# Performance work log

Hardware: AMD Instinct MI355X
Metric: run time of the kernel (lower is better)

The kernel has to match this reference:

```python
import jax, jax.numpy as jnp
import numpy as np

T, B, I, H = 1024, 64, 3, 2048


def setup_inputs() -> dict:
    key = jax.random.key(0)
    ks = jax.random.split(key, 6)
    lim = 1.0 / np.sqrt(H).astype(np.float32)  # eqx GRUCell init range
    return {
        "inp": jax.random.normal(ks[0], (T, B, I), jnp.float32),
        "init_hidden": jax.random.normal(ks[1], (B, H), jnp.float32),
        "weight_ih": jax.random.uniform(ks[2], (3 * H, I), jnp.float32, -lim, lim),
        "weight_hh": jax.random.uniform(ks[3], (3 * H, H), jnp.float32, -lim, lim),
        "bias": jax.random.uniform(ks[4], (3 * H,), jnp.float32, -lim, lim),
        "bias_n": jax.random.uniform(ks[5], (H,), jnp.float32, -lim, lim),
    }


def reference(inp, init_hidden, weight_ih, weight_hh, bias, bias_n):
    # Input projections for all timesteps at once: [T, B, 3H]
    igates_all = jnp.einsum("tbi,gi->tbg", inp, weight_ih) + bias

    def step(h, ig):
        hg = h @ weight_hh.T  # [B, 3H]
        ig_r, ig_z, ig_n = jnp.split(ig, 3, axis=-1)
        hg_r, hg_z, hg_n = jnp.split(hg, 3, axis=-1)
        reset = jax.nn.sigmoid(ig_r + hg_r)
        upd = jax.nn.sigmoid(ig_z + hg_z)
        new = jnp.tanh(ig_n + reset * (hg_n + bias_n))
        h_new = new + upd * (h - new)  # eqx GRUCell: new + inp_gate*(hidden-new)
        return h_new, h_new[:, 0]      # out = first hidden unit per step

    _, out = jax.lax.scan(step, init_hidden, igates_all)
    return out  # [T, B]
```

## Files before the change

kernel.cpp:

```cpp
#include <hip/hip_runtime.h>

typedef __attribute__((ext_vector_type(8))) short bf16x8;
typedef __attribute__((ext_vector_type(4))) float f32x4;
typedef __attribute__((ext_vector_type(4))) int i32x4;

#define Tn 1024
#define Bn 64
#define Hn 2048
#define NBLK 256
#define NTHR 512

#define GRP(ring, leaf, g) (((((ring) << 7) | ((leaf) << 3) | (g))) * 32)

#define SPIN_LIMIT (1u << 25)

__device__ __forceinline__ unsigned short f2b(float x) {
    unsigned u = __float_as_uint(x);
    return (unsigned short)((u + 0x7fffu + ((u >> 16) & 1u)) >> 16);
}
__device__ __forceinline__ float sigm(float x) {
    return __builtin_amdgcn_rcpf(1.0f + __expf(-x));
}
__device__ __forceinline__ float tanh_f(float x) {
    float e = __expf(2.0f * x);
    return 1.0f - 2.0f * __builtin_amdgcn_rcpf(1.0f + e);
}

__device__ __forceinline__ void store_short_wt(unsigned short* p, unsigned v) {
    asm volatile("global_store_short %0, %1, off sc0 sc1" :: "v"(p), "v"(v) : "memory");
}
__device__ __forceinline__ void store_dword_wt(float* p, float v) {
    asm volatile("global_store_dword %0, %1, off sc0 sc1" :: "v"(p), "v"(__float_as_uint(v)) : "memory");
}
__device__ __forceinline__ void store_u64_wt(unsigned long long* p, unsigned long long v) {
    asm volatile("global_store_dwordx2 %0, %1, off sc0 sc1" :: "v"(p), "v"(v) : "memory");
}
__device__ __forceinline__ unsigned poll_read(unsigned* p) {
    unsigned old;
    asm volatile("global_atomic_add %0, %1, %2, off sc0 sc1\n\ts_waitcnt vmcnt(0)"
                 : "=v"(old) : "v"(p), "v"(0u) : "memory");
    return old;
}

__device__ __forceinline__ long hfrag_off(int b, int k) {
    return ((long)(((k >> 5) * 4 + (b >> 4)) * 64) + ((k >> 3) & 3) * 16 + (b & 15)) * 8 + (k & 7);
}

__global__ void prep_kernel(const float* __restrict__ init_h,
                            unsigned short* __restrict__ h0,
                            unsigned* __restrict__ ctrl) {
    const int i = blockIdx.x * 256 + threadIdx.x;
    const int b  = i >> 9;
    const int k4 = (i & 511) << 2;
    float4 v = *reinterpret_cast<const float4*>(init_h + (long)b * Hn + k4);
    unsigned long long q = (unsigned long long)f2b(v.x)
                         | ((unsigned long long)f2b(v.y) << 16)
                         | ((unsigned long long)f2b(v.z) << 32)
                         | ((unsigned long long)f2b(v.w) << 48);
    store_u64_wt((unsigned long long*)(h0 + hfrag_off(b, k4)), q);
    if (i < 8192)
        asm volatile("global_store_dword %0, %1, off sc0 sc1"
                     :: "v"(ctrl + i), "v"(0u) : "memory");
}

__global__ void __launch_bounds__(NTHR, 2) gru_kernel(
    const float* __restrict__ inp,
    const float* __restrict__ init_h,
    const float* __restrict__ w_ih,
    const float* __restrict__ w_hh,
    const float* __restrict__ bias,
    const float* __restrict__ bias_n,
    unsigned short* __restrict__ h0,
    unsigned short* __restrict__ h1,
    unsigned* __restrict__ ctrl,
    float* __restrict__ out)
{
    __shared__ f32x4 red[2][4][2][3][64];

    const int tid  = threadIdx.x;
    const int lane = tid & 63;
    const int w    = tid >> 6;
    const int quad = lane >> 4;
    const int n16  = lane & 15;
    const int R    = blockIdx.x & 1;
    const int c    = blockIdx.x >> 1;
    const int jg   = c * 16 + n16;
    const int ks   = w * 256;
    const int bbase = 32 * R;

    bf16x8 Bf[3][8];
    #pragma unroll
    for (int nt = 0; nt < 3; ++nt) {
        const long row = (long)(nt * Hn + jg);
        #pragma unroll
        for (int k = 0; k < 8; ++k) {
            const float* p = w_hh + row * Hn + ks + k * 32 + quad * 8;
            bf16x8 b;
            #pragma unroll
            for (int j = 0; j < 8; ++j) b[j] = (short)f2b(p[j]);
            Bf[nt][k] = b;
        }
    }

    float wr0 = w_ih[jg*3+0], wr1 = w_ih[jg*3+1], wr2 = w_ih[jg*3+2];
    float wz0 = w_ih[(Hn+jg)*3+0], wz1 = w_ih[(Hn+jg)*3+1], wz2 = w_ih[(Hn+jg)*3+2];
    float wn0 = w_ih[(2*Hn+jg)*3+0], wn1 = w_ih[(2*Hn+jg)*3+1], wn2 = w_ih[(2*Hn+jg)*3+2];
    float br_ = bias[jg], bz_ = bias[Hn+jg], bn2_ = bias[2*Hn+jg];
    float bnn_ = bias_n[jg];

    float hst[4];
    if (w < 2) {
        #pragma unroll
        for (int r = 0; r < 4; ++r)
            hst[r] = init_h[(long)(bbase + 16 * w + quad * 4 + r) * Hn + jg];
    }

    const int kkE = c >> 1;
    const int qE  = (c & 1) * 2 + (n16 >> 3);
    const int eE  = n16 & 7;

    const int leafC = c >> 3;
    const int grp   = c >> 4;

    for (int t = 0; t < Tn; ++t) {
        const unsigned short* hcur = (t & 1) ? h1 : h0;
        unsigned short* hnext      = (t & 1) ? h0 : h1;
        f32x4 (*redp)[2][3][64] = red[t & 1];

        float xv[4][3];
        if (w < 2) {
            #pragma unroll
            for (int r = 0; r < 4; ++r) {
                const float* xp = inp + ((long)t * Bn + bbase + 16 * w + quad * 4 + r) * 3;
                xv[r][0] = xp[0]; xv[r][1] = xp[1]; xv[r][2] = xp[2];
            }
        }

        f32x4 acc[2][3];
        #pragma unroll
        for (int m = 0; m < 2; ++m)
            #pragma unroll
            for (int nt = 0; nt < 3; ++nt)
                acc[m][nt] = f32x4{0.f, 0.f, 0.f, 0.f};

        if (lane == 0 && t) {
            const unsigned tgt = (unsigned)(t << 5);
            unsigned spins = 0;
            while (poll_read(&ctrl[GRP(R, leafC, w)]) < tgt) {
                __builtin_amdgcn_s_sleep(1);
                if (++spins > SPIN_LIMIT) break;
            }
        }

        const unsigned short* pa = hcur + ((long)(32 * w + 2 * R) * 64 + lane) * 8;

        i32x4 hb[16];
        #pragma unroll
        for (int kki = 0; kki < 8; ++kki) {
            #pragma unroll
            for (int m = 0; m < 2; ++m) {
                asm volatile("global_load_dwordx4 %0, %1, off sc0 sc1"
                             : "=v"(hb[kki * 2 + m])
                             : "v"(pa + (long)(kki * 4 + m) * 512) : "memory");
            }
        }
        asm volatile("s_waitcnt vmcnt(0)"
                     : "+v"(hb[0]), "+v"(hb[1]), "+v"(hb[2]), "+v"(hb[3]),
                       "+v"(hb[4]), "+v"(hb[5]), "+v"(hb[6]), "+v"(hb[7]),
                       "+v"(hb[8]), "+v"(hb[9]), "+v"(hb[10]), "+v"(hb[11]),
                       "+v"(hb[12]), "+v"(hb[13]), "+v"(hb[14]), "+v"(hb[15])
                     :: "memory");
        __builtin_amdgcn_s_setprio(1);
        #pragma unroll
        for (int kki = 0; kki < 8; ++kki) {
            #pragma unroll
            for (int m = 0; m < 2; ++m) {
                union { i32x4 q; bf16x8 v; } u;
                u.q = hb[kki * 2 + m];
                bf16x8 a = u.v;
                acc[m][0] = __builtin_amdgcn_mfma_f32_16x16x32_bf16(a, Bf[0][kki], acc[m][0], 0, 0, 0);
                acc[m][1] = __builtin_amdgcn_mfma_f32_16x16x32_bf16(a, Bf[1][kki], acc[m][1], 0, 0, 0);
                acc[m][2] = __builtin_amdgcn_mfma_f32_16x16x32_bf16(a, Bf[2][kki], acc[m][2], 0, 0, 0);
            }
        }
        __builtin_amdgcn_s_setprio(0);

        if (w >= 4) {
            #pragma unroll
            for (int m = 0; m < 2; ++m)
                #pragma unroll
                for (int nt = 0; nt < 3; ++nt)
                    redp[w - 4][m][nt][lane] = acc[m][nt];
        }
        __syncthreads();
        if (w < 4) {
            f32x4 tmp[2][3];
            #pragma unroll
            for (int m = 0; m < 2; ++m)
                #pragma unroll
                for (int nt = 0; nt < 3; ++nt)
                    tmp[m][nt] = redp[w][m][nt][lane];
            #pragma unroll
            for (int m = 0; m < 2; ++m)
                #pragma unroll
                for (int nt = 0; nt < 3; ++nt)
                    redp[w][m][nt][lane] = acc[m][nt] + tmp[m][nt];
        }
        __syncthreads();

        if (w < 2) {
            f32x4 s0 = redp[0][w][0][lane], s1 = redp[0][w][1][lane], s2 = redp[0][w][2][lane];
            #pragma unroll
            for (int src = 1; src < 4; ++src) {
                s0 += redp[src][w][0][lane];
                s1 += redp[src][w][1][lane];
                s2 += redp[src][w][2][lane];
            }
            #pragma unroll
            for (int r = 0; r < 4; ++r) {
                const int b = bbase + 16 * w + quad * 4 + r;
                float pr = br_ + wr0*xv[r][0] + wr1*xv[r][1] + wr2*xv[r][2] + s0[r];
                float pz = bz_ + wz0*xv[r][0] + wz1*xv[r][1] + wz2*xv[r][2] + s1[r];
                float rr = sigm(pr);
                float zz = sigm(pz);
                float pn = bn2_ + wn0*xv[r][0] + wn1*xv[r][1] + wn2*xv[r][2] + rr * (s2[r] + bnn_);
                float nn = tanh_f(pn);
                float hv = nn + zz * (hst[r] - nn);
                hst[r] = hv;
                store_short_wt(hnext + ((long)((kkE * 4 + 2 * R + w) * 64) + qE * 16 + quad * 4 + r) * 8 + eE,
                               (unsigned)f2b(hv));
                if (c == 0 && n16 == 0)
                    store_dword_wt(out + t * Bn + b, hv);
            }
            asm volatile("s_waitcnt vmcnt(0)" ::: "memory");
            if (lane < 16)
                __hip_atomic_fetch_add(&ctrl[GRP(R, lane, grp)], 1u,
                                       __ATOMIC_RELAXED, __HIP_MEMORY_SCOPE_SYSTEM);
        }
    }
}

extern "C" void kernel_launch(void* const* d_in, const int* in_sizes, int n_in,
                              void* d_out, int out_size, void* d_ws, size_t ws_size,
                              hipStream_t stream) {
    const float* inp    = (const float*)d_in[0];
    const float* init_h = (const float*)d_in[1];
    const float* w_ih   = (const float*)d_in[2];
    const float* w_hh   = (const float*)d_in[3];
    const float* bias   = (const float*)d_in[4];
    const float* bias_n = (const float*)d_in[5];
    float* out = (float*)d_out;

    unsigned short* h0 = (unsigned short*)d_ws;
    unsigned short* h1 = h0 + 131072L;
    unsigned* ctrl     = (unsigned*)(h1 + 131072L);

    prep_kernel<<<128, 256, 0, stream>>>(init_h, h0, ctrl);
    gru_kernel<<<NBLK, NTHR, 0, stream>>>(inp, init_h, w_ih, w_hh, bias, bias_n,
                                          h0, h1, ctrl, out);
}
```

Baseline: 4.349 ms.

## Repartition GRU blocks to 32 hidden columns by 16 batch rows

```diff
diff --git a/kernel.cpp b/kernel.cpp
--- a/kernel.cpp
+++ b/kernel.cpp
@@ -10,7 +10,7 @@
 #define NBLK 256
 #define NTHR 512
 
-#define GRP(ring, leaf, g) (((((ring) << 7) | ((leaf) << 3) | (g))) * 32)
+#define GRP(ring, leaf, g) (((((ring) << 6) | ((leaf) << 3) | (g))) * 32)
 
 #define SPIN_LIMIT (1u << 25)
 
@@ -76,75 +76,65 @@
     float* __restrict__ out)
 {
     __shared__ f32x4 red[2][4][2][3][64];
+    __shared__ float xs[2][16][3];
 
     const int tid  = threadIdx.x;
     const int lane = tid & 63;
     const int w    = tid >> 6;
     const int quad = lane >> 4;
     const int n16  = lane & 15;
-    const int R    = blockIdx.x & 1;
-    const int c    = blockIdx.x >> 1;
-    const int jg   = c * 16 + n16;
+    const int R    = blockIdx.x & 3;
+    const int c    = blockIdx.x >> 2;
     const int ks   = w * 256;
-    const int bbase = 32 * R;
-
-    bf16x8 Bf[3][8];
+    const int bbase = 16 * R;
+
+    bf16x8 Bf[3][2][8];
     #pragma unroll
-    for (int nt = 0; nt < 3; ++nt) {
-        const long row = (long)(nt * Hn + jg);
-        #pragma unroll
-        for (int k = 0; k < 8; ++k) {
-            const float* p = w_hh + row * Hn + ks + k * 32 + quad * 8;
-            bf16x8 b;
-            #pragma unroll
-            for (int j = 0; j < 8; ++j) b[j] = (short)f2b(p[j]);
-            Bf[nt][k] = b;
+    for (int g = 0; g < 3; ++g) {
+        #pragma unroll
+        for (int nt = 0; nt < 2; ++nt) {
+            const long row = (long)(g * Hn + c * 32 + nt * 16 + n16);
+            #pragma unroll
+            for (int k = 0; k < 8; ++k) {
+                const float* p = w_hh + row * Hn + ks + k * 32 + quad * 8;
+                bf16x8 b;
+                #pragma unroll
+                for (int j = 0; j < 8; ++j) b[j] = (short)f2b(p[j]);
+                Bf[g][nt][k] = b;
+            }
         }
     }
-
-    float wr0 = w_ih[jg*3+0], wr1 = w_ih[jg*3+1], wr2 = w_ih[jg*3+2];
-    float wz0 = w_ih[(Hn+jg)*3+0], wz1 = w_ih[(Hn+jg)*3+1], wz2 = w_ih[(Hn+jg)*3+2];
-    float wn0 = w_ih[(2*Hn+jg)*3+0], wn1 = w_ih[(2*Hn+jg)*3+1], wn2 = w_ih[(2*Hn+jg)*3+2];
-    float br_ = bias[jg], bz_ = bias[Hn+jg], bn2_ = bias[2*Hn+jg];
-    float bnn_ = bias_n[jg];
 
     float hst[4];
     if (w < 2) {
+        const int jg = c * 32 + 16 * w + n16;
         #pragma unroll
         for (int r = 0; r < 4; ++r)
-            hst[r] = init_h[(long)(bbase + 16 * w + quad * 4 + r) * Hn + jg];
+            hst[r] = init_h[(long)(bbase + quad * 4 + r) * Hn + jg];
     }
 
-    const int kkE = c >> 1;
-    const int qE  = (c & 1) * 2 + (n16 >> 3);
-    const int eE  = n16 & 7;
-
     const int leafC = c >> 3;
-    const int grp   = c >> 4;
+    const int grp   = c >> 3;
 
     for (int t = 0; t < Tn; ++t) {
         const unsigned short* hcur = (t & 1) ? h1 : h0;
         unsigned short* hnext      = (t & 1) ? h0 : h1;
         f32x4 (*redp)[2][3][64] = red[t & 1];
 
-        float xv[4][3];
-        if (w < 2) {
-            #pragma unroll
-            for (int r = 0; r < 4; ++r) {
-                const float* xp = inp + ((long)t * Bn + bbase + 16 * w + quad * 4 + r) * 3;
-                xv[r][0] = xp[0]; xv[r][1] = xp[1]; xv[r][2] = xp[2];
-            }
+        if (w == 2 && lane < 48) {
+            const int row = lane / 3, col = lane % 3;
+            xs[t & 1][row][col] = inp[((long)t * Bn + bbase + row) * 3 + col];
         }
 
         f32x4 acc[2][3];
         #pragma unroll
-        for (int m = 0; m < 2; ++m)
-            #pragma unroll
-            for (int nt = 0; nt < 3; ++nt)
-                acc[m][nt] = f32x4{0.f, 0.f, 0.f, 0.f};
+        for (int nt = 0; nt < 2; ++nt)
+            #pragma unroll
+            for (int g = 0; g < 3; ++g)
+                acc[nt][g] = f32x4{0.f, 0.f, 0.f, 0.f};
 
         if (lane == 0 && t) {
-            const unsigned tgt = (unsigned)(t << 5);
+            const unsigned tgt = (unsigned)(t << 4);
             unsigned spins = 0;
             while (poll_read(&ctrl[GRP(R, leafC, w)]) < tgt) {
                 __builtin_amdgcn_s_sleep(1);
@@ -152,63 +142,69 @@
             }
         }
 
-        const unsigned short* pa = hcur + ((long)(32 * w + 2 * R) * 64 + lane) * 8;
-
-        i32x4 hb[16];
-        #pragma unroll
-        for (int kki = 0; kki < 8; ++kki) {
-            #pragma unroll
-            for (int m = 0; m < 2; ++m) {
+        const unsigned short* pa = hcur + ((long)((32 * w + R) * 64 + lane)) * 8;
+
+        i32x4 hb[4];
+        #pragma unroll
+        for (int half = 0; half < 2; ++half) {
+            #pragma unroll
+            for (int f = 0; f < 4; ++f) {
+                const int kki = half * 4 + f;
                 asm volatile("global_load_dwordx4 %0, %1, off sc0 sc1"
-                             : "=v"(hb[kki * 2 + m])
-                             : "v"(pa + (long)(kki * 4 + m) * 512) : "memory");
-            }
-        }
-        asm volatile("s_waitcnt vmcnt(0)"
-                     : "+v"(hb[0]), "+v"(hb[1]), "+v"(hb[2]), "+v"(hb[3]),
-                       "+v"(hb[4]), "+v"(hb[5]), "+v"(hb[6]), "+v"(hb[7]),
-                       "+v"(hb[8]), "+v"(hb[9]), "+v"(hb[10]), "+v"(hb[11]),
-                       "+v"(hb[12]), "+v"(hb[13]), "+v"(hb[14]), "+v"(hb[15])
-                     :: "memory");
-        __builtin_amdgcn_s_setprio(1);
-        #pragma unroll
-        for (int kki = 0; kki < 8; ++kki) {
-            #pragma unroll
-            for (int m = 0; m < 2; ++m) {
+                             : "=v"(hb[f]) : "v"(pa + (long)kki * 2048) : "memory");
+            }
+            asm volatile("s_waitcnt vmcnt(0)"
+                         : "+v"(hb[0]), "+v"(hb[1]), "+v"(hb[2]), "+v"(hb[3])
+                         :: "memory");
+            __builtin_amdgcn_s_setprio(1);
+            #pragma unroll
+            for (int f = 0; f < 4; ++f) {
+                const int kki = half * 4 + f;
                 union { i32x4 q; bf16x8 v; } u;
-                u.q = hb[kki * 2 + m];
+                u.q = hb[f];
                 bf16x8 a = u.v;
-                acc[m][0] = __builtin_amdgcn_mfma_f32_16x16x32_bf16(a, Bf[0][kki], acc[m][0], 0, 0, 0);
-                acc[m][1] = __builtin_amdgcn_mfma_f32_16x16x32_bf16(a, Bf[1][kki], acc[m][1], 0, 0, 0);
-                acc[m][2] = __builtin_amdgcn_mfma_f32_16x16x32_bf16(a, Bf[2][kki], acc[m][2], 0, 0, 0);
-            }
-        }
-        __builtin_amdgcn_s_setprio(0);
+                #pragma unroll
+                for (int nt = 0; nt < 2; ++nt) {
+                    acc[nt][0] = __builtin_amdgcn_mfma_f32_16x16x32_bf16(a, Bf[0][nt][kki], acc[nt][0], 0, 0, 0);
+                    acc[nt][1] = __builtin_amdgcn_mfma_f32_16x16x32_bf16(a, Bf[1][nt][kki], acc[nt][1], 0, 0, 0);
+                    acc[nt][2] = __builtin_amdgcn_mfma_f32_16x16x32_bf16(a, Bf[2][nt][kki], acc[nt][2], 0, 0, 0);
+                }
+            }
+            __builtin_amdgcn_s_setprio(0);
+            __builtin_amdgcn_sched_barrier(0);
+        }
 
         if (w >= 4) {
             #pragma unroll
-            for (int m = 0; m < 2; ++m)
-                #pragma unroll
-                for (int nt = 0; nt < 3; ++nt)
-                    redp[w - 4][m][nt][lane] = acc[m][nt];
+            for (int nt = 0; nt < 2; ++nt)
+                #pragma unroll
+                for (int g = 0; g < 3; ++g)
+                    redp[w - 4][nt][g][lane] = acc[nt][g];
         }
         __syncthreads();
         if (w < 4) {
             f32x4 tmp[2][3];
             #pragma unroll
-            for (int m = 0; m < 2; ++m)
-                #pragma unroll
-                for (int nt = 0; nt < 3; ++nt)
-                    tmp[m][nt] = redp[w][m][nt][lane];
-            #pragma unroll
-            for (int m = 0; m < 2; ++m)
-                #pragma unroll
-                for (int nt = 0; nt < 3; ++nt)
-                    redp[w][m][nt][lane] = acc[m][nt] + tmp[m][nt];
+            for (int nt = 0; nt < 2; ++nt)
+                #pragma unroll
+                for (int g = 0; g < 3; ++g)
+                    tmp[nt][g] = redp[w][nt][g][lane];
+            #pragma unroll
+            for (int nt = 0; nt < 2; ++nt)
+                #pragma unroll
+                for (int g = 0; g < 3; ++g)
+                    redp[w][nt][g][lane] = acc[nt][g] + tmp[nt][g];
         }
         __syncthreads();
 
         if (w < 2) {
+            const int jg = c * 32 + 16 * w + n16;
+            float wr0 = w_ih[jg*3+0], wr1 = w_ih[jg*3+1], wr2 = w_ih[jg*3+2];
+            float wz0 = w_ih[(Hn+jg)*3+0], wz1 = w_ih[(Hn+jg)*3+1], wz2 = w_ih[(Hn+jg)*3+2];
+            float wn0 = w_ih[(2*Hn+jg)*3+0], wn1 = w_ih[(2*Hn+jg)*3+1], wn2 = w_ih[(2*Hn+jg)*3+2];
+            float br_ = bias[jg], bz_ = bias[Hn+jg], bn2_ = bias[2*Hn+jg];
+            float bnn_ = bias_n[jg];
+
             f32x4 s0 = redp[0][w][0][lane], s1 = redp[0][w][1][lane], s2 = redp[0][w][2][lane];
             #pragma unroll
             for (int src = 1; src < 4; ++src) {
@@ -216,9 +212,16 @@
                 s1 += redp[src][w][1][lane];
                 s2 += redp[src][w][2][lane];
             }
+            float xv[4][3];
             #pragma unroll
             for (int r = 0; r < 4; ++r) {
-                const int b = bbase + 16 * w + quad * 4 + r;
+                xv[r][0] = xs[t & 1][quad * 4 + r][0];
+                xv[r][1] = xs[t & 1][quad * 4 + r][1];
+                xv[r][2] = xs[t & 1][quad * 4 + r][2];
+            }
+            #pragma unroll
+            for (int r = 0; r < 4; ++r) {
+                const int b = bbase + quad * 4 + r;
                 float pr = br_ + wr0*xv[r][0] + wr1*xv[r][1] + wr2*xv[r][2] + s0[r];
                 float pz = bz_ + wz0*xv[r][0] + wz1*xv[r][1] + wz2*xv[r][2] + s1[r];
                 float rr = sigm(pr);
@@ -227,13 +230,14 @@
                 float nn = tanh_f(pn);
                 float hv = nn + zz * (hst[r] - nn);
                 hst[r] = hv;
-                store_short_wt(hnext + ((long)((kkE * 4 + 2 * R + w) * 64) + qE * 16 + quad * 4 + r) * 8 + eE,
+                store_short_wt(hnext + ((long)((c * 4 + R) * 64)
+                                        + (2 * w + (n16 >> 3)) * 16 + quad * 4 + r) * 8 + (n16 & 7),
                                (unsigned)f2b(hv));
-                if (c == 0 && n16 == 0)
+                if (w == 0 && c == 0 && n16 == 0)
                     store_dword_wt(out + t * Bn + b, hv);
             }
             asm volatile("s_waitcnt vmcnt(0)" ::: "memory");
-            if (lane < 16)
+            if (lane < 8)
                 __hip_atomic_fetch_add(&ctrl[GRP(R, lane, grp)], 1u,
                                        __ATOMIC_RELAXED, __HIP_MEMORY_SCOPE_SYSTEM);
         }
```

Measured after the change: 9.828 ms. 126% more time.
